# Kernel optimization log

Hardware: AMD Instinct MI355X
Metric: run time of the kernel (lower is better)

## Reference

```python
import jax, jax.numpy as jnp
import numpy as np

N_NODES = 100000
N_CAND = 32768
HIDDEN = 1024
N_REL = 10


def setup_inputs() -> dict:
    key = jax.random.key(0)
    k0, k1, k2, k3, k4, k5 = jax.random.split(key, 6)
    node_embeddings = jax.random.normal(k0, (N_NODES, HIDDEN), dtype=jnp.float32)
    src_idx = jax.random.randint(k1, (N_CAND,), 0, N_NODES, dtype=jnp.int32)
    dst_idx = jax.random.randint(k2, (N_CAND,), 0, N_NODES, dtype=jnp.int32)
    labels = jax.random.randint(k3, (N_CAND,), 0, N_REL, dtype=jnp.int32)
    # Linear weights stored as [in, out] so forward is x @ W + b
    W1 = jax.random.normal(k4, (4 * HIDDEN, HIDDEN), dtype=jnp.float32) * (1.0 / np.sqrt(4 * HIDDEN))
    b1 = jnp.zeros((HIDDEN,), dtype=jnp.float32)
    W2 = jax.random.normal(k5, (HIDDEN, N_REL), dtype=jnp.float32) * (1.0 / np.sqrt(HIDDEN))
    b2 = jnp.zeros((N_REL,), dtype=jnp.float32)
    return {"node_embeddings": node_embeddings, "src_idx": src_idx, "dst_idx": dst_idx,
            "labels": labels, "W1": W1, "b1": b1, "W2": W2, "b2": b2}


def reference(node_embeddings, src_idx, dst_idx, labels, W1, b1, W2, b2):
    # Vectorized gather of candidate endpoints (replaces Python loop)
    src = node_embeddings[src_idx]            # [C, H]
    dst = node_embeddings[dst_idx]            # [C, H]
    feats = jnp.concatenate([src, dst, jnp.abs(src - dst), src * dst], axis=-1)  # [C, 4H]
    h = jax.nn.gelu(feats @ W1 + b1, approximate=False)  # exact GELU, matches torch default
    # Dropout is identity in eval mode
    logits = h @ W2 + b2                      # [C, n_rel]
    logp = jax.nn.log_softmax(logits, axis=-1)
    loss = -jnp.mean(jnp.take_along_axis(logp, labels[:, None].astype(jnp.int32), axis=-1))
    return loss, logits
```

## Files before the change

### kernel.cpp

```cpp
#include <hip/hip_runtime.h>
#include <stdint.h>

#define CANDS 32768
#define HID   1024
#define KDIM  4096
#define NREL  10

typedef __attribute__((ext_vector_type(8))) short bf16x8;
typedef __attribute__((ext_vector_type(4))) float f32x4;

__device__ __forceinline__ float bf2f(unsigned short u) {
  union { unsigned int i; float f; } v; v.i = ((unsigned int)u) << 16; return v.f;
}
__device__ __forceinline__ unsigned short f2bf(float f) {
  union { float f; unsigned int i; } v; v.f = f;
  unsigned int x = v.i;
  return (unsigned short)((x + 0x7FFFu + ((x >> 16) & 1u)) >> 16);
}
__device__ __forceinline__ void async16(const void* g, void* l) {
  __builtin_amdgcn_global_load_lds(
      (const __attribute__((address_space(1))) unsigned int*)(uintptr_t)g,
      (__attribute__((address_space(3))) unsigned int*)(uintptr_t)l,
      16, 0, 0);
}

__global__ void transpose_w1(const float* __restrict__ W1,
                             unsigned short* __restrict__ W1T) {
  __shared__ __align__(16) unsigned short tile[64][72];
  int bk = blockIdx.x;
  int bn = blockIdx.y;
  int t = threadIdx.x;
  int r = t >> 3, c8 = (t & 7) * 8;
  for (int i = 0; i < 2; ++i) {
    int rr = r + i * 32;
    const float4* src = (const float4*)(W1 + (size_t)(bk * 64 + rr) * HID + bn * 64 + c8);
    float4 v0 = src[0], v1 = src[1];
    tile[rr][c8 + 0] = f2bf(v0.x); tile[rr][c8 + 1] = f2bf(v0.y);
    tile[rr][c8 + 2] = f2bf(v0.z); tile[rr][c8 + 3] = f2bf(v0.w);
    tile[rr][c8 + 4] = f2bf(v1.x); tile[rr][c8 + 5] = f2bf(v1.y);
    tile[rr][c8 + 6] = f2bf(v1.z); tile[rr][c8 + 7] = f2bf(v1.w);
  }
  __syncthreads();
  for (int i = 0; i < 2; ++i) {
    int rr = r + i * 32;
    unsigned short tmp[8];
    for (int j = 0; j < 8; ++j) tmp[j] = tile[c8 + j][rr];
    ushort4* dst = (ushort4*)(W1T + (size_t)(bn * 64 + rr) * KDIM + bk * 64 + c8);
    dst[0] = *(ushort4*)&tmp[0];
    dst[1] = *(ushort4*)&tmp[4];
  }
}

__global__ __launch_bounds__(256) void build_feats(
    const float* __restrict__ emb,
    const int* __restrict__ sidx,
    const int* __restrict__ didx,
    unsigned short* __restrict__ feats) {
  int t = threadIdx.x;
  for (int m = blockIdx.x; m < CANDS; m += gridDim.x) {
    const float* srow = emb + (size_t)sidx[m] * HID;
    const float* drow = emb + (size_t)didx[m] * HID;
    float4 s4 = *(const float4*)(srow + t * 4);
    float4 d4 = *(const float4*)(drow + t * 4);
    unsigned short* o = feats + (size_t)m * KDIM;
    ushort4 sv, dv, av, pv;
    sv.x = f2bf(s4.x); sv.y = f2bf(s4.y); sv.z = f2bf(s4.z); sv.w = f2bf(s4.w);
    dv.x = f2bf(d4.x); dv.y = f2bf(d4.y); dv.z = f2bf(d4.z); dv.w = f2bf(d4.w);
    av.x = f2bf(fabsf(s4.x - d4.x)); av.y = f2bf(fabsf(s4.y - d4.y));
    av.z = f2bf(fabsf(s4.z - d4.z)); av.w = f2bf(fabsf(s4.w - d4.w));
    pv.x = f2bf(s4.x * d4.x); pv.y = f2bf(s4.y * d4.y);
    pv.z = f2bf(s4.z * d4.z); pv.w = f2bf(s4.w * d4.w);
    *(ushort4*)(o + t * 4)           = sv;
    *(ushort4*)(o + HID + t * 4)     = dv;
    *(ushort4*)(o + 2 * HID + t * 4) = av;
    *(ushort4*)(o + 3 * HID + t * 4) = pv;
  }
}

#define BM 128
#define BN 128
#define BK 32
__global__ __launch_bounds__(256) void gemm1_gelu(
    const unsigned short* __restrict__ A,
    const unsigned short* __restrict__ BT,
    const float* __restrict__ b1,
    unsigned short* __restrict__ H) {
  __shared__ __align__(16) unsigned short laA[BM * BK];
  __shared__ __align__(16) unsigned short laB[BN * BK];
  int bid = blockIdx.x;
  int xcd = bid & 7;
  int s   = bid >> 3;
  int m_tile = xcd * 32 + (s >> 3);
  int n_tile = s & 7;
  int m0 = m_tile * BM;
  int n0 = n_tile * BN;

  int t = threadIdx.x;
  int lane = t & 63;
  int wave = t >> 6;
  int wrow = (wave >> 1) * 64, wcol = (wave & 1) * 64;
  int quad = lane >> 4, l16 = lane & 15;

  f32x4 acc[4][4] = {};

  int srow = t >> 2;
  int scol = (t & 3) * 8;
  const unsigned short* gA0 = A  + (size_t)(m0 + srow) * KDIM + scol;
  const unsigned short* gA1 = A  + (size_t)(m0 + srow + 64) * KDIM + scol;
  const unsigned short* gB0 = BT + (size_t)(n0 + srow) * KDIM + scol;
  const unsigned short* gB1 = BT + (size_t)(n0 + srow + 64) * KDIM + scol;
  unsigned short* lA0 = &laA[srow * BK + scol];
  unsigned short* lA1 = &laA[(srow + 64) * BK + scol];
  unsigned short* lB0 = &laB[srow * BK + scol];
  unsigned short* lB1 = &laB[(srow + 64) * BK + scol];

  for (int kk = 0; kk < KDIM; kk += BK) {
    async16(gA0 + kk, lA0);
    async16(gA1 + kk, lA1);
    async16(gB0 + kk, lB0);
    async16(gB1 + kk, lB1);
    __syncthreads();
    bf16x8 af[4], bfr[4];
#pragma unroll
    for (int i = 0; i < 4; ++i)
      af[i] = *(const bf16x8*)&laA[(wrow + i * 16 + l16) * BK + quad * 8];
#pragma unroll
    for (int j = 0; j < 4; ++j)
      bfr[j] = *(const bf16x8*)&laB[(wcol + j * 16 + l16) * BK + quad * 8];
#pragma unroll
    for (int i = 0; i < 4; ++i)
#pragma unroll
      for (int j = 0; j < 4; ++j)
        acc[i][j] = __builtin_amdgcn_mfma_f32_16x16x32_bf16(af[i], bfr[j], acc[i][j], 0, 0, 0);
    __syncthreads();
  }
#pragma unroll
  for (int j = 0; j < 4; ++j) {
    int n = n0 + wcol + j * 16 + l16;
    float bias = b1[n];
#pragma unroll
    for (int i = 0; i < 4; ++i) {
#pragma unroll
      for (int r = 0; r < 4; ++r) {
        int m = m0 + wrow + i * 16 + quad * 4 + r;
        float x = acc[i][j][r] + bias;
        float g = 0.5f * x * (1.0f + erff(x * 0.70710678118654752f));
        H[(size_t)m * HID + n] = f2bf(g);
      }
    }
  }
}

__global__ __launch_bounds__(256) void gemm2_loss(
    const unsigned short* __restrict__ H,
    const float* __restrict__ W2,
    const float* __restrict__ b2,
    const int* __restrict__ labels,
    float* __restrict__ out,
    float* __restrict__ gacc) {
#define W2P 1032
  __shared__ __align__(16) unsigned short w2t[16 * W2P];
  __shared__ float lacc;
  int t = threadIdx.x;
  int lane = t & 63, wave = t >> 6;
  int quad = lane >> 4, l16 = lane & 15;
  if (t == 0) lacc = 0.0f;
  for (int k = t; k < HID; k += 256) {
    for (int j = 0; j < NREL; ++j) w2t[j * W2P + k] = f2bf(W2[(size_t)k * NREL + j]);
    for (int j = NREL; j < 16; ++j) w2t[j * W2P + k] = 0;
  }
  __syncthreads();

  int r0 = blockIdx.x * 64 + wave * 16;
  const unsigned short* hrow = H + (size_t)(r0 + l16) * HID;
  f32x4 acc = {};
#pragma unroll 8
  for (int s = 0; s < 32; ++s) {
    bf16x8 a = *(const bf16x8*)(hrow + s * 32 + quad * 8);
    bf16x8 b = *(const bf16x8*)&w2t[l16 * W2P + s * 32 + quad * 8];
    acc = __builtin_amdgcn_mfma_f32_16x16x32_bf16(a, b, acc, 0, 0, 0);
  }

  int col = l16;
  float bias = (col < NREL) ? b2[col] : 0.0f;
  float local = 0.0f;
#pragma unroll
  for (int r = 0; r < 4; ++r) {
    int row = r0 + quad * 4 + r;
    float x = acc[r] + bias;
    float v = (col < NREL) ? x : -1e30f;
    float mx = v;
    for (int d = 1; d < 16; d <<= 1) mx = fmaxf(mx, __shfl_xor(mx, d));
    float e = (col < NREL) ? expf(x - mx) : 0.0f;
    float se = e;
    for (int d = 1; d < 16; d <<= 1) se += __shfl_xor(se, d);
    float lse = mx + logf(se);
    if (col < NREL) {
      out[1 + (size_t)row * NREL + col] = x;
      if (labels[row] == col) local += (lse - x);
    }
  }
  atomicAdd(&lacc, local);
  __syncthreads();
  if (t == 0) atomicAdd(gacc, lacc);
}

__global__ void finalize_loss(const float* __restrict__ gacc, float* __restrict__ out) {
  out[0] = *gacc * (1.0f / (float)CANDS);
}

extern "C" void kernel_launch(void* const* d_in, const int* in_sizes, int n_in,
                              void* d_out, int out_size, void* d_ws, size_t ws_size,
                              hipStream_t stream) {
  const float* emb    = (const float*)d_in[0];
  const int*   sidx   = (const int*)d_in[1];
  const int*   didx   = (const int*)d_in[2];
  const int*   labels = (const int*)d_in[3];
  const float* W1     = (const float*)d_in[4];
  const float* b1     = (const float*)d_in[5];
  const float* W2     = (const float*)d_in[6];
  const float* b2     = (const float*)d_in[7];
  float* out = (float*)d_out;

  char* ws = (char*)d_ws;
  float*          gacc  = (float*)ws;
  unsigned short* W1T   = (unsigned short*)(ws + 256);
  unsigned short* feats = (unsigned short*)(ws + 256 + 8388608);
  unsigned short* H     = (unsigned short*)(ws + 256 + 8388608 + 268435456);

  hipMemsetAsync(gacc, 0, sizeof(float), stream);
  transpose_w1<<<dim3(64, 16), 256, 0, stream>>>(W1, W1T);
  build_feats<<<2048, 256, 0, stream>>>(emb, sidx, didx, feats);
  gemm1_gelu<<<2048, 256, 0, stream>>>(feats, W1T, b1, H);
  gemm2_loss<<<CANDS / 64, 256, 0, stream>>>(H, W2, b2, labels, out, gacc);
  finalize_loss<<<1, 1, 0, stream>>>(gacc, out);
}
```

Before: 949.2 us.

## Double GEMM1 K-tile to 64 with XOR-swizzled LDS layout

The K tile of the main GEMM grows from 32 to 64, so each iteration issues twice as many MFMAs per pair of barriers and halves the number of sync points. The LDS tiles use an XOR swizzle on 16-byte chunks, applied on the global side of the async global-to-LDS loads and again on the fragment reads, to avoid bank conflicts with the wider 128-byte rows. The feature-building kernel also gets twice as many blocks. The costs are doubled LDS use per block and more address arithmetic, and the loop is still single-buffered with no overlap between loads and compute.

```diff
diff --git a/kernel.cpp b/kernel.cpp
--- a/kernel.cpp
+++ b/kernel.cpp
@@ -79,7 +79,7 @@
 
 #define BM 128
 #define BN 128
-#define BK 32
+#define BK 64
 __global__ __launch_bounds__(256) void gemm1_gelu(
     const unsigned short* __restrict__ A,
     const unsigned short* __restrict__ BT,
@@ -103,35 +103,44 @@
 
   f32x4 acc[4][4] = {};
 
-  int srow = t >> 2;
-  int scol = (t & 3) * 8;
-  const unsigned short* gA0 = A  + (size_t)(m0 + srow) * KDIM + scol;
-  const unsigned short* gA1 = A  + (size_t)(m0 + srow + 64) * KDIM + scol;
-  const unsigned short* gB0 = BT + (size_t)(n0 + srow) * KDIM + scol;
-  const unsigned short* gB1 = BT + (size_t)(n0 + srow + 64) * KDIM + scol;
-  unsigned short* lA0 = &laA[srow * BK + scol];
-  unsigned short* lA1 = &laA[(srow + 64) * BK + scol];
-  unsigned short* lB0 = &laB[srow * BK + scol];
-  unsigned short* lB1 = &laB[(srow + 64) * BK + scol];
+  int srow = t >> 3;
+  int cpos = t & 7;
+  int gchunk = cpos ^ (srow & 7);
+  const unsigned short* gA = A  + (size_t)(m0 + srow) * KDIM + gchunk * 8;
+  const unsigned short* gB = BT + (size_t)(n0 + srow) * KDIM + gchunk * 8;
+  unsigned short* lA = &laA[srow * BK + cpos * 8];
+  unsigned short* lB = &laB[srow * BK + cpos * 8];
+  const size_t rstep = (size_t)32 * KDIM;
+  const int    lstep = 32 * BK;
 
   for (int kk = 0; kk < KDIM; kk += BK) {
-    async16(gA0 + kk, lA0);
-    async16(gA1 + kk, lA1);
-    async16(gB0 + kk, lB0);
-    async16(gB1 + kk, lB1);
+#pragma unroll
+    for (int i = 0; i < 4; ++i) {
+      async16(gA + i * rstep + kk, lA + i * lstep);
+      async16(gB + i * rstep + kk, lB + i * lstep);
+    }
     __syncthreads();
-    bf16x8 af[4], bfr[4];
-#pragma unroll
-    for (int i = 0; i < 4; ++i)
-      af[i] = *(const bf16x8*)&laA[(wrow + i * 16 + l16) * BK + quad * 8];
-#pragma unroll
-    for (int j = 0; j < 4; ++j)
-      bfr[j] = *(const bf16x8*)&laB[(wcol + j * 16 + l16) * BK + quad * 8];
-#pragma unroll
-    for (int i = 0; i < 4; ++i)
-#pragma unroll
-      for (int j = 0; j < 4; ++j)
-        acc[i][j] = __builtin_amdgcn_mfma_f32_16x16x32_bf16(af[i], bfr[j], acc[i][j], 0, 0, 0);
+#pragma unroll
+    for (int ks = 0; ks < 2; ++ks) {
+      bf16x8 af[4], bfr[4];
+#pragma unroll
+      for (int i = 0; i < 4; ++i) {
+        int r = wrow + i * 16 + l16;
+        int p = (ks * 4 + quad) ^ (r & 7);
+        af[i] = *(const bf16x8*)&laA[r * BK + p * 8];
+      }
+#pragma unroll
+      for (int j = 0; j < 4; ++j) {
+        int r = wcol + j * 16 + l16;
+        int p = (ks * 4 + quad) ^ (r & 7);
+        bfr[j] = *(const bf16x8*)&laB[r * BK + p * 8];
+      }
+#pragma unroll
+      for (int i = 0; i < 4; ++i)
+#pragma unroll
+        for (int j = 0; j < 4; ++j)
+          acc[i][j] = __builtin_amdgcn_mfma_f32_16x16x32_bf16(af[i], bfr[j], acc[i][j], 0, 0, 0);
+    }
     __syncthreads();
   }
 #pragma unroll
@@ -230,7 +239,7 @@
 
   hipMemsetAsync(gacc, 0, sizeof(float), stream);
   transpose_w1<<<dim3(64, 16), 256, 0, stream>>>(W1, W1T);
-  build_feats<<<2048, 256, 0, stream>>>(emb, sidx, didx, feats);
+  build_feats<<<4096, 256, 0, stream>>>(emb, sidx, didx, feats);
   gemm1_gelu<<<2048, 256, 0, stream>>>(feats, W1T, b1, H);
   gemm2_loss<<<CANDS / 64, 256, 0, stream>>>(H, W2, b2, labels, out, gacc);
   finalize_loss<<<1, 1, 0, stream>>>(gacc, out);
```

New measurement: 980.9 us. +3.3%, slower.
